# Performance work log

Hardware: AMD Instinct MI355X
Metric: run time of the kernel (lower is better)

The kernel has to match this reference:

```python
import jax, jax.numpy as jnp
import numpy as np

B, C, T = 16, 256, 8192
TF, HID, HEADS, HD, K = 512, 256, 8, 32, 2
EPS = 1e-6


def setup_inputs() -> dict:
    key = jax.random.key(0)
    ks = jax.random.split(key, 8)
    s = 0.02  # small init scale for weight matrices
    return {
        "x": jax.random.normal(ks[0], (B, C, 1, T), jnp.float32),
        "temb": jax.random.normal(ks[1], (B, TF), jnp.float32),
        "ln_w": jnp.ones((C,), jnp.float32),
        "ln_b": jnp.zeros((C,), jnp.float32),
        "ss_w": jax.random.normal(ks[2], (2 * C, TF), jnp.float32) * s,
        "ss_b": jnp.zeros((2 * C,), jnp.float32),
        "kv_w": jax.random.normal(ks[3], (2 * HID, C), jnp.float32) * s,
        "kv_b": jnp.zeros((2 * HID,), jnp.float32),
        "q": jax.random.normal(ks[4], (HEADS, HD), jnp.float32),
        "qt_w": jax.random.normal(ks[5], (HID, TF), jnp.float32) * s,
        "qt_b": jnp.zeros((HID,), jnp.float32),
        "rpe": jax.random.normal(ks[6], (HEADS, K), jnp.float32) * s,
        "proj_w": jax.random.normal(ks[7], (HID, HID), jnp.float32) * s,
        "proj_b": jnp.zeros((HID,), jnp.float32),
    }


def reference(x, temb, ln_w, ln_b, ss_w, ss_b, kv_w, kv_b, q, qt_w, qt_b, rpe, proj_w, proj_b):
    b, c, h, w = x.shape  # h == 1, w == T
    # --- LayerNorm2d: normalize over channel dim ---
    xt = jnp.transpose(x, (0, 2, 3, 1))  # [B,H,W,C]
    mu = jnp.mean(xt, axis=-1, keepdims=True)
    var = jnp.mean(jnp.square(xt - mu), axis=-1, keepdims=True)
    xn = (xt - mu) * jax.lax.rsqrt(var + EPS) * ln_w + ln_b
    xn = jnp.transpose(xn, (0, 3, 1, 2))  # [B,C,H,W]
    # --- ShiftAndScale (FiLM): SiLU -> Linear -> chunk ---
    cond = jax.nn.silu(temb) @ ss_w.T + ss_b  # [B, 2C]
    shift, scale = jnp.split(cond, 2, axis=1)
    xm = xn * (1.0 + scale[:, :, None, None]) + shift[:, :, None, None]
    # --- FusedQnA1d: learned-query windowed attention downsample (k=2, s=2) ---
    t = h * w
    t2 = t // K
    xf = xm.reshape(b, c, t)
    kv = jnp.einsum('bct,dc->bdt', xf, kv_w) + kv_b[None, :, None]  # [B,2*HID,T]
    kk, vv = jnp.split(kv, 2, axis=1)
    kk = kk.reshape(b, HEADS, HD, t2, K)  # non-overlapping stride-2 windows
    vv = vv.reshape(b, HEADS, HD, t2, K)
    # learned query, offset by timestep-conditioned query (use_timestep_query=True)
    qt = (jax.nn.silu(temb) @ qt_w.T + qt_b).reshape(b, HEADS, HD)
    qb = q[None] + qt  # [B,HEADS,HD]
    logits = jnp.einsum('bhd,bhdtw->bhtw', qb, kk) * (HD ** -0.5) + rpe[None, :, None, :]
    attn = jax.nn.softmax(logits, axis=-1)
    o = jnp.einsum('bhtw,bhdtw->bhdt', attn, vv).reshape(b, HID, t2)
    out = jnp.einsum('bct,dc->bdt', o, proj_w) + proj_b[None, :, None]
    return out.reshape(b, HID, h, w // K)
```

## Files before the change

### kernel.cpp

```cpp
#include <hip/hip_runtime.h>
#include <hip/hip_bf16.h>

#define Bn 16
#define Cn 256
#define Tn 8192
#define TFn 512
#define HIDn 256
#define HEADSn 8
#define HDn 32
#define T2n (Tn/2)
#define TW 256
#define T2W 128
#define XPAD 264
#define CKP 72

#define XSWZ(row) ((((row) >> 3) & 7) << 3)

#define WS_CS   0
#define WS_CC   4096
#define WS_CQ   8192
#define WS_G    12288
#define WS_H    16384
#define WS_QKB  20480
#define WS_QA   20608
#define WS_QH   20736
#define WS_AV   20864
#define WS_BV   24960
#define WS_BF16 29056
#define BF_QKW2 0
#define BF_WV2  65536
#define BF_PROJ 1114112

typedef __attribute__((ext_vector_type(8))) __bf16 bf16x8;
typedef __attribute__((ext_vector_type(4))) __bf16 bf16x4;
typedef __attribute__((ext_vector_type(4))) float f32x4;

__global__ __launch_bounds__(256)
void prepA_kernel(const float* __restrict__ temb,
                  const float* __restrict__ ss_w, const float* __restrict__ ss_b,
                  const float* __restrict__ qt_w, const float* __restrict__ qt_b,
                  const float* __restrict__ qw, float* __restrict__ ws)
{
    const int p = blockIdx.x;
    const int b = blockIdx.y;
    const int tid = threadIdx.x, lane = tid & 63, w = tid >> 6;
    __shared__ float st[TFn];
    for (int i = tid; i < TFn; i += 256) {
        float v = temb[b*TFn + i];
        st[i] = v / (1.f + __expf(-v));
    }
    __syncthreads();
    float4 s1 = *(const float4*)&st[lane*8];
    float4 s2 = *(const float4*)&st[lane*8 + 4];
    for (int i = 0; i < 16; ++i) {
        int row = p*64 + w*16 + i;
        const float* W = (row < 2*Cn) ? (ss_w + (size_t)row*TFn)
                                      : (qt_w + (size_t)(row - 2*Cn)*TFn);
        float4 a = *(const float4*)&W[lane*8];
        float4 c = *(const float4*)&W[lane*8 + 4];
        float d = a.x*s1.x + a.y*s1.y + a.z*s1.z + a.w*s1.w
                + c.x*s2.x + c.y*s2.y + c.z*s2.z + c.w*s2.w;
        #pragma unroll
        for (int off = 1; off < 64; off <<= 1) d += __shfl_xor(d, off);
        if (lane == 0) {
            if (row < Cn)
                ws[WS_CS + b*Cn + row] = d + ss_b[row];
            else if (row < 2*Cn)
                ws[WS_CC + b*Cn + (row - Cn)] = d + ss_b[row];
            else
                ws[WS_CQ + b*Cn + (row - 2*Cn)] = d + qt_b[row - 2*Cn] + qw[row - 2*Cn];
        }
    }
}

__global__ __launch_bounds__(256)
void prepB_kernel(const float* __restrict__ ln_w, const float* __restrict__ ln_b,
                  const float* __restrict__ kv_w, const float* __restrict__ kv_b,
                  float* __restrict__ ws)
{
    const int b = blockIdx.x, tid = threadIdx.x;
    __bf16* bfr = (__bf16*)(ws + WS_BF16);
    __shared__ float qbs[HIDn], gs[Cn], hs[Cn];
    __shared__ float pA[4][8], pH[4][8];
    const int c = tid, wv = tid >> 6, ln = tid & 63;

    float sc1 = 1.f + ws[WS_CC + b*Cn + c];
    float g = ln_w[c] * sc1;
    float h = ln_b[c] * sc1 + ws[WS_CS + b*Cn + c];
    gs[c] = g; hs[c] = h;
    ws[WS_G + b*Cn + c] = g;
    ws[WS_H + b*Cn + c] = h;
    qbs[c] = ws[WS_CQ + b*Cn + c];
    __syncthreads();

    __bf16* qkw2B = bfr + BF_QKW2 + b*16*Cn;
    for (int hh2 = 0; hh2 < HEADSn; ++hh2) {
        float accq = 0.f;
        #pragma unroll
        for (int d = 0; d < HDn; ++d)
            accq += qbs[hh2*HDn + d] * kv_w[(size_t)(hh2*HDn + d)*Cn + c];
        float wg = accq * gs[c];
        float wh = accq * hs[c];
        qkw2B[hh2*Cn + c] = (__bf16)wg;
        float ra = wg, rh = wh;
        #pragma unroll
        for (int off = 1; off < 64; off <<= 1) {
            ra += __shfl_xor(ra, off);
            rh += __shfl_xor(rh, off);
        }
        if (ln == 0) { pA[wv][hh2] = ra; pH[wv][hh2] = rh; }
    }
    for (int i = tid; i < 8*Cn; i += 256) qkw2B[8*Cn + i] = (__bf16)0.f;
    __syncthreads();
    if (tid < HEADSn) {
        ws[WS_QA + b*8 + tid] = pA[0][tid]+pA[1][tid]+pA[2][tid]+pA[3][tid];
        ws[WS_QH + b*8 + tid] = pH[0][tid]+pH[1][tid]+pH[2][tid]+pH[3][tid];
        float accb = 0.f;
        #pragma unroll
        for (int d = 0; d < HDn; ++d) accb += qbs[tid*HDn + d]*kv_b[tid*HDn + d];
        ws[WS_QKB + b*8 + tid] = accb;
    }
}

__global__ __launch_bounds__(256)
void prep2_kernel(const float* __restrict__ kv_w, const float* __restrict__ kv_b,
                  const float* __restrict__ proj_w, float* __restrict__ ws)
{
    const int tid = threadIdx.x, blk = blockIdx.x;
    __bf16* bfr = (__bf16*)(ws + WS_BF16);
    if (blk < 256) {
        int b  = blk >> 4, ch = blk & 15;
        int rr = tid >> 4, jj = tid & 15;
        int d  = ch*16 + rr;
        const float* gb = ws + WS_G + b*Cn;
        const float* hb = ws + WS_H + b*Cn;
        const float* wrow = kv_w + (size_t)(Cn + d)*Cn;
        __bf16* dst = bfr + BF_WV2 + (size_t)b*Cn*Cn + (size_t)d*Cn;
        float sa = 0.f, sb = 0.f;
        #pragma unroll
        for (int kk = 0; kk < 2; ++kk) {
            bf16x8 pk;
            #pragma unroll
            for (int j = 0; j < 8; ++j) {
                int cc = jj*16 + kk*8 + j;
                float v = wrow[cc], g = gb[cc];
                float vg = v*g;
                pk[j] = (__bf16)vg;
                sa += vg;
                sb += v*hb[cc];
            }
            *(bf16x8*)&dst[jj*16 + kk*8] = pk;
        }
        #pragma unroll
        for (int off = 1; off < 16; off <<= 1) {
            sa += __shfl_xor(sa, off);
            sb += __shfl_xor(sb, off);
        }
        if (jj == 0) {
            ws[WS_AV + b*Cn + d] = sa;
            ws[WS_BV + b*Cn + d] = sb + kv_b[Cn + d];
        }
    } else {
        size_t i0 = (size_t)(blk - 256)*4096 + (size_t)tid*16;
        #pragma unroll
        for (int kk = 0; kk < 2; ++kk) {
            bf16x8 pk;
            #pragma unroll
            for (int j = 0; j < 8; ++j) pk[j] = (__bf16)proj_w[i0 + kk*8 + j];
            *(bf16x8*)&bfr[BF_PROJ + i0 + kk*8] = pk;
        }
    }
}

__global__ __launch_bounds__(512, 2)
void qna_main(const float* __restrict__ x, const float* __restrict__ rpe,
              const float* __restrict__ proj_b,
              const float* __restrict__ ws, float* __restrict__ out)
{
    __shared__ __bf16 xcb[2][TW][CKP];
    __shared__ float spool[4096];
    __shared__ float ivs[TW], mivs[TW];
    __shared__ float AvS[Cn], BvS[Cn], pbs[Cn];
    __shared__ float qAs[8], qHs[8], qkbs2[8];
    __shared__ float rpes[8][2];

    const int tid  = threadIdx.x;
    const int bt   = blockIdx.x;
    const int b    = blockIdx.y;
    const int lane = tid & 63;
    const int w    = tid >> 6;
    const int r    = lane & 15;
    const int qq   = lane >> 4;

    const __bf16* bfr   = (const __bf16*)(ws + WS_BF16);
    const __bf16* qkw2B = bfr + BF_QKW2 + b*16*Cn;
    const __bf16* Wv2B  = bfr + BF_WV2 + (size_t)b*Cn*Cn;
    const __bf16* projB = bfr + BF_PROJ;

    if (tid < 256) {
        AvS[tid] = ws[WS_AV + b*Cn + tid];
        BvS[tid] = ws[WS_BV + b*Cn + tid];
    } else {
        int t2 = tid - 256;
        pbs[t2] = proj_b[t2];
        if (t2 < 8) {
            qAs[t2]   = ws[WS_QA + b*8 + t2];
            qHs[t2]   = ws[WS_QH + b*8 + t2];
            qkbs2[t2] = ws[WS_QKB + b*8 + t2];
        }
        if (t2 >= 16 && t2 < 32) rpes[(t2-16)>>1][t2&1] = rpe[t2-16];
    }

    const size_t xbase = (size_t)b*Cn*Tn + (size_t)bt*TW + 4*lane;
    const int tL = 4*lane;
    float4 v[8];
    float4 s4 = {0,0,0,0}, q4 = {0,0,0,0};

    auto stage_write = [&](int BUF) {
        #pragma unroll
        for (int i = 0; i < 8; ++i) {
            s4.x += v[i].x; s4.y += v[i].y; s4.z += v[i].z; s4.w += v[i].w;
            q4.x += v[i].x*v[i].x; q4.y += v[i].y*v[i].y;
            q4.z += v[i].z*v[i].z; q4.w += v[i].w*v[i].w;
        }
        #pragma unroll
        for (int j = 0; j < 4; ++j) {
            int t = tL + j;
            bf16x8 pk;
            pk[0]=(__bf16)((const float*)&v[0])[j]; pk[1]=(__bf16)((const float*)&v[1])[j];
            pk[2]=(__bf16)((const float*)&v[2])[j]; pk[3]=(__bf16)((const float*)&v[3])[j];
            pk[4]=(__bf16)((const float*)&v[4])[j]; pk[5]=(__bf16)((const float*)&v[5])[j];
            pk[6]=(__bf16)((const float*)&v[6])[j]; pk[7]=(__bf16)((const float*)&v[7])[j];
            *(bf16x8*)&xcb[BUF][t][(8*w) ^ XSWZ(t)] = pk;
        }
    };

    #pragma unroll
    for (int i = 0; i < 8; ++i)
        v[i] = *(const float4*)&x[xbase + (size_t)(8*w + i)*Tn];
    stage_write(0);
    __syncthreads();

    f32x4 accL[2];
    accL[0] = (f32x4){0.f,0.f,0.f,0.f};
    accL[1] = (f32x4){0.f,0.f,0.f,0.f};
    f32x4 acc[4][8];
    #pragma unroll
    for (int m = 0; m < 4; ++m)
        #pragma unroll
        for (int n = 0; n < 8; ++n) acc[m][n] = (f32x4){0.f,0.f,0.f,0.f};
    const int d0 = (w & 3) * 64;
    const int tb = (w >> 2) * 128;

    #pragma unroll
    for (int ch = 0; ch < 4; ++ch) {
        const int cur = ch & 1;
        if (ch < 3) {
            #pragma unroll
            for (int i = 0; i < 8; ++i)
                v[i] = *(const float4*)&x[xbase + (size_t)((ch+1)*64 + 8*w + i)*Tn];
        }
        #pragma unroll
        for (int k0 = 0; k0 < 2; ++k0) {
            const int kc = ch*64 + k0*32 + qq*8;
            const int cl = (k0*32 + qq*8);
            bf16x8 aQ = *(const bf16x8*)&qkw2B[(size_t)r*Cn + kc];
            #pragma unroll
            for (int u = 0; u < 2; ++u) {
                const int trow = (2*w + u)*16 + r;
                bf16x8 bq = *(const bf16x8*)&xcb[cur][trow][cl ^ XSWZ(trow)];
                accL[u] = __builtin_amdgcn_mfma_f32_16x16x32_bf16(aQ, bq, accL[u], 0, 0, 0);
            }
            bf16x8 bb[8];
            #pragma unroll
            for (int n = 0; n < 8; ++n) {
                const int row = tb + n*16 + r;
                bb[n] = *(const bf16x8*)&xcb[cur][row][cl ^ XSWZ(row)];
            }
            #pragma unroll
            for (int m = 0; m < 4; ++m) {
                bf16x8 a = *(const bf16x8*)&Wv2B[(size_t)(d0 + m*16 + r)*Cn + kc];
                #pragma unroll
                for (int n = 0; n < 8; ++n)
                    acc[m][n] = __builtin_amdgcn_mfma_f32_16x16x32_bf16(a, bb[n], acc[m][n], 0, 0, 0);
            }
        }
        if (ch < 3) {
            __syncthreads();
            stage_write(cur ^ 1);
            if (ch == 2) {
                spool[0*512 + w*64 + lane] = s4.x;
                spool[1*512 + w*64 + lane] = s4.y;
                spool[2*512 + w*64 + lane] = s4.z;
                spool[3*512 + w*64 + lane] = s4.w;
                spool[2048 + 0*512 + w*64 + lane] = q4.x;
                spool[2048 + 1*512 + w*64 + lane] = q4.y;
                spool[2048 + 2*512 + w*64 + lane] = q4.z;
                spool[2048 + 3*512 + w*64 + lane] = q4.w;
            }
            __syncthreads();
        }
    }

    __syncthreads();
    if (tid < 256) {
        const int t = tid, comp = t & 3, lq = t >> 2;
        float s = 0.f, sq = 0.f;
        #pragma unroll
        for (int w2 = 0; w2 < 8; ++w2) {
            s  += spool[comp*512 + w2*64 + lq];
            sq += spool[2048 + comp*512 + w2*64 + lq];
        }
        float mean = s * (1.f/Cn);
        float var  = sq * (1.f/Cn) - mean*mean;
        float iv   = rsqrtf(var + 1e-6f);
        ivs[t]  = iv;
        mivs[t] = mean * iv;
    }
    __syncthreads();

    float* aw = spool;
    {
        const float sc = 0.17677669529663687f;
        #pragma unroll
        for (int u = 0; u < 2; ++u) {
            const int tcol = (2*w + u)*16 + r;
            float iv = ivs[tcol], miv = mivs[tcol];
            #pragma unroll
            for (int rr = 0; rr < 4; ++rr) {
                int h  = (qq*4 + rr) & 7;
                float l = (accL[u][rr]*iv - miv*qAs[h] + qHs[h] + qkbs2[h])*sc + rpes[h][r&1];
                float mx = fmaxf(l, __shfl_xor(l, 1));
                float e  = __expf(l - mx);
                float sm = e + __shfl_xor(e, 1);
                float aval = e / sm;
                if (qq < 2) aw[(qq*4 + rr)*256 + tcol] = aval;
            }
        }
    }
    __syncthreads();

    __bf16* oTp = &xcb[0][0][0];
    {
        #pragma unroll
        for (int m = 0; m < 4; ++m) {
            const int dbase = d0 + m*16 + qq*4;
            const int h = dbase >> 5;
            float av4[4], bv4[4];
            #pragma unroll
            for (int rr = 0; rr < 4; ++rr) { av4[rr] = AvS[dbase+rr]; bv4[rr] = BvS[dbase+rr]; }
            #pragma unroll
            for (int n = 0; n < 8; ++n) {
                const int tl = tb + n*16 + r;
                float ivn = ivs[tl], mivn = mivs[tl];
                float a0 = aw[h*256 + (tl & ~1)], a1 = aw[h*256 + (tl | 1)];
                bf16x4 ov;
                #pragma unroll
                for (int rr = 0; rr < 4; ++rr) {
                    float vv = ivn*acc[m][n][rr] - mivn*av4[rr] + bv4[rr];
                    float vo = __shfl_xor(vv, 1);
                    float o  = a0*vv + a1*vo;
                    ov[rr] = (__bf16)o;
                }
                if (!(r & 1)) {
                    int u = (tb >> 1) + n*8 + (r >> 1);
                    *(bf16x4*)&oTp[(size_t)u*XPAD + dbase] = ov;
                }
            }
        }
    }
    __syncthreads();

    const int t2b = (w >> 2) * 64;
    f32x4 acc2[4][4];
    #pragma unroll
    for (int m = 0; m < 4; ++m)
        #pragma unroll
        for (int n = 0; n < 4; ++n) acc2[m][n] = (f32x4){0.f,0.f,0.f,0.f};
    #pragma unroll
    for (int k0 = 0; k0 < 8; ++k0) {
        bf16x8 bb2[4];
        #pragma unroll
        for (int n = 0; n < 4; ++n)
            bb2[n] = *(const bf16x8*)&oTp[(size_t)(t2b + n*16 + r)*XPAD + k0*32 + qq*8];
        #pragma unroll
        for (int m = 0; m < 4; ++m) {
            bf16x8 a = *(const bf16x8*)&projB[(size_t)(d0 + m*16 + r)*Cn + k0*32 + qq*8];
            #pragma unroll
            for (int n = 0; n < 4; ++n)
                acc2[m][n] = __builtin_amdgcn_mfma_f32_16x16x32_bf16(a, bb2[n], acc2[m][n], 0, 0, 0);
        }
    }

    {
        float* ob = out + (size_t)b*HIDn*T2n + (size_t)bt*T2W;
        #pragma unroll
        for (int m = 0; m < 4; ++m) {
            #pragma unroll
            for (int n = 0; n < 4; ++n) {
                #pragma unroll
                for (int rr = 0; rr < 4; ++rr) {
                    int e = d0 + m*16 + qq*4 + rr;
                    ob[(size_t)e*T2n + t2b + n*16 + r] = acc2[m][n][rr] + pbs[e];
                }
            }
        }
    }
}

extern "C" void kernel_launch(void* const* d_in, const int* in_sizes, int n_in,
                              void* d_out, int out_size, void* d_ws, size_t ws_size,
                              hipStream_t stream) {
    (void)in_sizes; (void)n_in; (void)out_size; (void)ws_size;
    const float* x      = (const float*)d_in[0];
    const float* temb   = (const float*)d_in[1];
    const float* ln_w   = (const float*)d_in[2];
    const float* ln_b   = (const float*)d_in[3];
    const float* ss_w   = (const float*)d_in[4];
    const float* ss_b   = (const float*)d_in[5];
    const float* kv_w   = (const float*)d_in[6];
    const float* kv_b   = (const float*)d_in[7];
    const float* q      = (const float*)d_in[8];
    const float* qt_w   = (const float*)d_in[9];
    const float* qt_b   = (const float*)d_in[10];
    const float* rpe    = (const float*)d_in[11];
    const float* proj_w = (const float*)d_in[12];
    const float* proj_b = (const float*)d_in[13];
    float* ws  = (float*)d_ws;
    float* out = (float*)d_out;

    prepA_kernel<<<dim3(12, Bn), dim3(256), 0, stream>>>(
        temb, ss_w, ss_b, qt_w, qt_b, q, ws);
    prepB_kernel<<<dim3(Bn), dim3(256), 0, stream>>>(ln_w, ln_b, kv_w, kv_b, ws);
    prep2_kernel<<<dim3(272), dim3(256), 0, stream>>>(kv_w, kv_b, proj_w, ws);
    qna_main<<<dim3(Tn/TW, Bn), dim3(512), 0, stream>>>(x, rpe, proj_b, ws, out);
}
```

Measured before the change: 111.6 us.

## Split fused attention kernel into stage-1 and projection kernels via workspace

```diff
diff --git a/kernel.cpp b/kernel.cpp
--- a/kernel.cpp
+++ b/kernel.cpp
@@ -13,8 +13,10 @@
 #define T2W 128
 #define XPAD 264
 #define CKP 72
-
-#define XSWZ(row) ((((row) >> 3) & 7) << 3)
+#define S1TW 128
+
+#define XSWZ(row)   ((((row) >> 3) & 7) << 3)
+#define XSWZ32(row) ((((row) >> 3) & 3) << 3)
 
 #define WS_CS   0
 #define WS_CC   4096
@@ -30,6 +32,8 @@
 #define BF_QKW2 0
 #define BF_WV2  65536
 #define BF_PROJ 1114112
+#define WS_OG   618880
+#define WS_NEED 36029952ull
 
 typedef __attribute__((ext_vector_type(8))) __bf16 bf16x8;
 typedef __attribute__((ext_vector_type(4))) __bf16 bf16x4;
@@ -168,6 +172,244 @@
             #pragma unroll
             for (int j = 0; j < 8; ++j) pk[j] = (__bf16)proj_w[i0 + kk*8 + j];
             *(bf16x8*)&bfr[BF_PROJ + i0 + kk*8] = pk;
+        }
+    }
+}
+
+__global__ __launch_bounds__(256, 2)
+void qna_stage1(const float* __restrict__ x, const float* __restrict__ rpe,
+                float* __restrict__ ws)
+{
+    __shared__ __bf16 xcb[2][S1TW][40];
+    __shared__ float sp_s[4*128], sp_q[4*128];
+    __shared__ float ivs[S1TW], mivs[S1TW];
+    __shared__ float aw[8*128];
+    __shared__ __bf16 oTb[64][264];
+    __shared__ float AvS[Cn], BvS[Cn];
+    __shared__ float qAs[8], qHs[8], qkbs2[8];
+    __shared__ float rpes[8][2];
+
+    const int tid  = threadIdx.x;
+    const int bt   = blockIdx.x;
+    const int b    = blockIdx.y;
+    const int lane = tid & 63;
+    const int w    = tid >> 6;
+    const int r    = lane & 15;
+    const int qq   = lane >> 4;
+
+    const __bf16* bfr   = (const __bf16*)(ws + WS_BF16);
+    const __bf16* qkw2B = bfr + BF_QKW2 + b*16*Cn;
+    const __bf16* Wv2B  = bfr + BF_WV2 + (size_t)b*Cn*Cn;
+    __bf16* oG = (__bf16*)(ws + WS_OG) + ((size_t)b*T2n + (size_t)bt*64)*Cn;
+
+    AvS[tid] = ws[WS_AV + b*Cn + tid];
+    BvS[tid] = ws[WS_BV + b*Cn + tid];
+    if (tid < 8) {
+        qAs[tid]   = ws[WS_QA + b*8 + tid];
+        qHs[tid]   = ws[WS_QH + b*8 + tid];
+        qkbs2[tid] = ws[WS_QKB + b*8 + tid];
+    }
+    if (tid >= 16 && tid < 32) rpes[(tid-16)>>1][tid&1] = rpe[tid-16];
+
+    const size_t xbase = (size_t)b*Cn*Tn + (size_t)bt*S1TW + 2*lane;
+    const int t0 = 2*lane;
+    float2 v[8];
+    float s0 = 0.f, s1 = 0.f, q0 = 0.f, q1 = 0.f;
+
+    auto stage_write = [&](int BUF) {
+        bf16x8 p0, p1;
+        #pragma unroll
+        for (int i = 0; i < 8; ++i) {
+            s0 += v[i].x; q0 += v[i].x*v[i].x;
+            s1 += v[i].y; q1 += v[i].y*v[i].y;
+            p0[i] = (__bf16)v[i].x;
+            p1[i] = (__bf16)v[i].y;
+        }
+        *(bf16x8*)&xcb[BUF][t0][(8*w) ^ XSWZ32(t0)]     = p0;
+        *(bf16x8*)&xcb[BUF][t0+1][(8*w) ^ XSWZ32(t0+1)] = p1;
+    };
+
+    #pragma unroll
+    for (int i = 0; i < 8; ++i)
+        v[i] = *(const float2*)&x[xbase + (size_t)(8*w + i)*Tn];
+    stage_write(0);
+    __syncthreads();
+
+    f32x4 accL[2];
+    accL[0] = (f32x4){0.f,0.f,0.f,0.f};
+    accL[1] = (f32x4){0.f,0.f,0.f,0.f};
+    f32x4 acc[4][8];
+    #pragma unroll
+    for (int m = 0; m < 4; ++m)
+        #pragma unroll
+        for (int n = 0; n < 8; ++n) acc[m][n] = (f32x4){0.f,0.f,0.f,0.f};
+    const int d0 = w * 64;
+
+    #pragma unroll
+    for (int ch = 0; ch < 8; ++ch) {
+        const int cur = ch & 1;
+        if (ch < 7) {
+            #pragma unroll
+            for (int i = 0; i < 8; ++i)
+                v[i] = *(const float2*)&x[xbase + (size_t)((ch+1)*32 + 8*w + i)*Tn];
+        }
+        const int kc = ch*32 + qq*8;
+        const int cl = qq*8;
+        {
+            bf16x8 aQ = *(const bf16x8*)&qkw2B[(size_t)r*Cn + kc];
+            #pragma unroll
+            for (int u = 0; u < 2; ++u) {
+                const int trow = (2*w + u)*16 + r;
+                bf16x8 bq = *(const bf16x8*)&xcb[cur][trow][cl ^ XSWZ32(trow)];
+                accL[u] = __builtin_amdgcn_mfma_f32_16x16x32_bf16(aQ, bq, accL[u], 0, 0, 0);
+            }
+        }
+        {
+            bf16x8 bb[8];
+            #pragma unroll
+            for (int n = 0; n < 8; ++n) {
+                const int row = n*16 + r;
+                bb[n] = *(const bf16x8*)&xcb[cur][row][cl ^ XSWZ32(row)];
+            }
+            #pragma unroll
+            for (int m = 0; m < 4; ++m) {
+                bf16x8 a = *(const bf16x8*)&Wv2B[(size_t)(d0 + m*16 + r)*Cn + kc];
+                #pragma unroll
+                for (int n = 0; n < 8; ++n)
+                    acc[m][n] = __builtin_amdgcn_mfma_f32_16x16x32_bf16(a, bb[n], acc[m][n], 0, 0, 0);
+            }
+        }
+        if (ch < 7) {
+            __syncthreads();
+            stage_write(cur ^ 1);
+            if (ch == 6) {
+                sp_s[w*128 + t0]     = s0;
+                sp_s[w*128 + t0 + 1] = s1;
+                sp_q[w*128 + t0]     = q0;
+                sp_q[w*128 + t0 + 1] = q1;
+            }
+            __syncthreads();
+        }
+    }
+
+    if (tid < S1TW) {
+        float s = sp_s[tid] + sp_s[128+tid] + sp_s[256+tid] + sp_s[384+tid];
+        float sq = sp_q[tid] + sp_q[128+tid] + sp_q[256+tid] + sp_q[384+tid];
+        float mean = s * (1.f/Cn);
+        float var  = sq * (1.f/Cn) - mean*mean;
+        float iv   = rsqrtf(var + 1e-6f);
+        ivs[tid]  = iv;
+        mivs[tid] = mean * iv;
+    }
+    __syncthreads();
+
+    {
+        const float sc = 0.17677669529663687f;
+        #pragma unroll
+        for (int u = 0; u < 2; ++u) {
+            const int tcol = (2*w + u)*16 + r;
+            float iv = ivs[tcol], miv = mivs[tcol];
+            #pragma unroll
+            for (int rr = 0; rr < 4; ++rr) {
+                int h  = (qq*4 + rr) & 7;
+                float l = (accL[u][rr]*iv - miv*qAs[h] + qHs[h] + qkbs2[h])*sc + rpes[h][r&1];
+                float mx = fmaxf(l, __shfl_xor(l, 1));
+                float e  = __expf(l - mx);
+                float sm = e + __shfl_xor(e, 1);
+                float aval = e / sm;
+                if (qq < 2) aw[(qq*4 + rr)*128 + tcol] = aval;
+            }
+        }
+    }
+    __syncthreads();
+
+    {
+        #pragma unroll
+        for (int m = 0; m < 4; ++m) {
+            const int dbase = d0 + m*16 + qq*4;
+            const int h = dbase >> 5;
+            float av4[4], bv4[4];
+            #pragma unroll
+            for (int rr = 0; rr < 4; ++rr) { av4[rr] = AvS[dbase+rr]; bv4[rr] = BvS[dbase+rr]; }
+            #pragma unroll
+            for (int n = 0; n < 8; ++n) {
+                const int tl = n*16 + r;
+                float ivn = ivs[tl], mivn = mivs[tl];
+                float a0 = aw[h*128 + (tl & ~1)], a1 = aw[h*128 + (tl | 1)];
+                bf16x4 ov;
+                #pragma unroll
+                for (int rr = 0; rr < 4; ++rr) {
+                    float vv = ivn*acc[m][n][rr] - mivn*av4[rr] + bv4[rr];
+                    float vo = __shfl_xor(vv, 1);
+                    float o  = a0*vv + a1*vo;
+                    ov[rr] = (__bf16)o;
+                }
+                if (!(r & 1)) {
+                    int u = n*8 + (r >> 1);
+                    *(bf16x4*)&oTb[u][dbase] = ov;
+                }
+            }
+        }
+    }
+    __syncthreads();
+
+    {
+        int u = tid >> 2, seg = tid & 3;
+        const __bf16* src = &oTb[u][seg*64];
+        __bf16* dst = oG + (size_t)u*Cn + seg*64;
+        #pragma unroll
+        for (int k = 0; k < 8; ++k)
+            *(bf16x8*)&dst[k*8] = *(const bf16x8*)&src[k*8];
+    }
+}
+
+__global__ __launch_bounds__(256, 2)
+void qna_proj(const float* __restrict__ ws, const float* __restrict__ proj_b,
+              float* __restrict__ out)
+{
+    const int tid  = threadIdx.x;
+    const int bt   = blockIdx.x;
+    const int b    = blockIdx.y;
+    const int lane = tid & 63;
+    const int w    = tid >> 6;
+    const int r    = lane & 15;
+    const int qq   = lane >> 4;
+
+    const __bf16* projB = (const __bf16*)(ws + WS_BF16) + BF_PROJ;
+    const __bf16* oG = (const __bf16*)(ws + WS_OG) + ((size_t)b*T2n + (size_t)bt*128)*Cn;
+    const int e0 = w * 64;
+
+    f32x4 acc[4][8];
+    #pragma unroll
+    for (int m = 0; m < 4; ++m)
+        #pragma unroll
+        for (int n = 0; n < 8; ++n) acc[m][n] = (f32x4){0.f,0.f,0.f,0.f};
+
+    #pragma unroll
+    for (int k0 = 0; k0 < 8; ++k0) {
+        bf16x8 bb[8];
+        #pragma unroll
+        for (int n = 0; n < 8; ++n)
+            bb[n] = *(const bf16x8*)&oG[(size_t)(n*16 + r)*Cn + k0*32 + qq*8];
+        #pragma unroll
+        for (int m = 0; m < 4; ++m) {
+            bf16x8 a = *(const bf16x8*)&projB[(size_t)(e0 + m*16 + r)*Cn + k0*32 + qq*8];
+            #pragma unroll
+            for (int n = 0; n < 8; ++n)
+                acc[m][n] = __builtin_amdgcn_mfma_f32_16x16x32_bf16(a, bb[n], acc[m][n], 0, 0, 0);
+        }
+    }
+
+    float* ob = out + (size_t)b*HIDn*T2n + (size_t)bt*128;
+    #pragma unroll
+    for (int m = 0; m < 4; ++m) {
+        #pragma unroll
+        for (int rr = 0; rr < 4; ++rr) {
+            int e = e0 + m*16 + qq*4 + rr;
+            float pb = proj_b[e];
+            #pragma unroll
+            for (int n = 0; n < 8; ++n)
+                ob[(size_t)e*T2n + n*16 + r] = acc[m][n][rr] + pb;
         }
     }
 }
@@ -411,7 +653,7 @@
 extern "C" void kernel_launch(void* const* d_in, const int* in_sizes, int n_in,
                               void* d_out, int out_size, void* d_ws, size_t ws_size,
                               hipStream_t stream) {
-    (void)in_sizes; (void)n_in; (void)out_size; (void)ws_size;
+    (void)in_sizes; (void)n_in; (void)out_size;
     const float* x      = (const float*)d_in[0];
     const float* temb   = (const float*)d_in[1];
     const float* ln_w   = (const float*)d_in[2];
@@ -433,5 +675,11 @@
         temb, ss_w, ss_b, qt_w, qt_b, q, ws);
     prepB_kernel<<<dim3(Bn), dim3(256), 0, stream>>>(ln_w, ln_b, kv_w, kv_b, ws);
     prep2_kernel<<<dim3(272), dim3(256), 0, stream>>>(kv_w, kv_b, proj_w, ws);
-    qna_main<<<dim3(Tn/TW, Bn), dim3(512), 0, stream>>>(x, rpe, proj_b, ws, out);
+
+    if (ws_size >= WS_NEED) {
+        qna_stage1<<<dim3(Tn/S1TW, Bn), dim3(256), 0, stream>>>(x, rpe, ws);
+        qna_proj<<<dim3(T2n/128, Bn), dim3(256), 0, stream>>>(ws, proj_b, out);
+    } else {
+        qna_main<<<dim3(Tn/TW, Bn), dim3(512), 0, stream>>>(x, rpe, proj_b, ws, out);
+    }
 }
```

New measurement: 148.9 us. +33.4%, slower.

## Deepen x-load prefetch to two chunks and halve per-chunk barriers

Applied to the files above, without the earlier changes.

```diff
diff --git a/kernel.cpp b/kernel.cpp
--- a/kernel.cpp
+++ b/kernel.cpp
@@ -213,32 +213,59 @@
 
     const size_t xbase = (size_t)b*Cn*Tn + (size_t)bt*TW + 4*lane;
     const int tL = 4*lane;
-    float4 v[8];
+    float4 vA[4], vB[4];
     float4 s4 = {0,0,0,0}, q4 = {0,0,0,0};
 
-    auto stage_write = [&](int BUF) {
-        #pragma unroll
-        for (int i = 0; i < 8; ++i) {
-            s4.x += v[i].x; s4.y += v[i].y; s4.z += v[i].z; s4.w += v[i].w;
-            q4.x += v[i].x*v[i].x; q4.y += v[i].y*v[i].y;
-            q4.z += v[i].z*v[i].z; q4.w += v[i].w*v[i].w;
+    auto issueA = [&](int ch) {
+        #pragma unroll
+        for (int i = 0; i < 4; ++i)
+            vA[i] = *(const float4*)&x[xbase + (size_t)(ch*64 + 8*w + i)*Tn];
+    };
+    auto issueB = [&](int ch) {
+        #pragma unroll
+        for (int i = 0; i < 4; ++i)
+            vB[i] = *(const float4*)&x[xbase + (size_t)(ch*64 + 8*w + 4 + i)*Tn];
+    };
+    auto stageA = [&](int BUF) {
+        #pragma unroll
+        for (int i = 0; i < 4; ++i) {
+            s4.x += vA[i].x; s4.y += vA[i].y; s4.z += vA[i].z; s4.w += vA[i].w;
+            q4.x += vA[i].x*vA[i].x; q4.y += vA[i].y*vA[i].y;
+            q4.z += vA[i].z*vA[i].z; q4.w += vA[i].w*vA[i].w;
         }
         #pragma unroll
         for (int j = 0; j < 4; ++j) {
             int t = tL + j;
-            bf16x8 pk;
-            pk[0]=(__bf16)((const float*)&v[0])[j]; pk[1]=(__bf16)((const float*)&v[1])[j];
-            pk[2]=(__bf16)((const float*)&v[2])[j]; pk[3]=(__bf16)((const float*)&v[3])[j];
-            pk[4]=(__bf16)((const float*)&v[4])[j]; pk[5]=(__bf16)((const float*)&v[5])[j];
-            pk[6]=(__bf16)((const float*)&v[6])[j]; pk[7]=(__bf16)((const float*)&v[7])[j];
-            *(bf16x8*)&xcb[BUF][t][(8*w) ^ XSWZ(t)] = pk;
+            bf16x4 pk;
+            pk[0] = (__bf16)((const float*)&vA[0])[j];
+            pk[1] = (__bf16)((const float*)&vA[1])[j];
+            pk[2] = (__bf16)((const float*)&vA[2])[j];
+            pk[3] = (__bf16)((const float*)&vA[3])[j];
+            *(bf16x4*)&xcb[BUF][t][(8*w) ^ XSWZ(t)] = pk;
         }
     };
-
-    #pragma unroll
-    for (int i = 0; i < 8; ++i)
-        v[i] = *(const float4*)&x[xbase + (size_t)(8*w + i)*Tn];
-    stage_write(0);
+    auto stageB = [&](int BUF) {
+        #pragma unroll
+        for (int i = 0; i < 4; ++i) {
+            s4.x += vB[i].x; s4.y += vB[i].y; s4.z += vB[i].z; s4.w += vB[i].w;
+            q4.x += vB[i].x*vB[i].x; q4.y += vB[i].y*vB[i].y;
+            q4.z += vB[i].z*vB[i].z; q4.w += vB[i].w*vB[i].w;
+        }
+        #pragma unroll
+        for (int j = 0; j < 4; ++j) {
+            int t = tL + j;
+            bf16x4 pk;
+            pk[0] = (__bf16)((const float*)&vB[0])[j];
+            pk[1] = (__bf16)((const float*)&vB[1])[j];
+            pk[2] = (__bf16)((const float*)&vB[2])[j];
+            pk[3] = (__bf16)((const float*)&vB[3])[j];
+            *(bf16x4*)&xcb[BUF][t][((8*w) ^ XSWZ(t)) + 4] = pk;
+        }
+    };
+
+    issueA(0); issueB(0);
+    stageA(0); stageB(0);
+    issueA(1); issueB(1);
     __syncthreads();
 
     f32x4 accL[2];
@@ -256,38 +283,10 @@
     for (int ch = 0; ch < 4; ++ch) {
         const int cur = ch & 1;
         if (ch < 3) {
-            #pragma unroll
-            for (int i = 0; i < 8; ++i)
-                v[i] = *(const float4*)&x[xbase + (size_t)((ch+1)*64 + 8*w + i)*Tn];
-        }
-        #pragma unroll
-        for (int k0 = 0; k0 < 2; ++k0) {
-            const int kc = ch*64 + k0*32 + qq*8;
-            const int cl = (k0*32 + qq*8);
-            bf16x8 aQ = *(const bf16x8*)&qkw2B[(size_t)r*Cn + kc];
-            #pragma unroll
-            for (int u = 0; u < 2; ++u) {
-                const int trow = (2*w + u)*16 + r;
-                bf16x8 bq = *(const bf16x8*)&xcb[cur][trow][cl ^ XSWZ(trow)];
-                accL[u] = __builtin_amdgcn_mfma_f32_16x16x32_bf16(aQ, bq, accL[u], 0, 0, 0);
-            }
-            bf16x8 bb[8];
-            #pragma unroll
-            for (int n = 0; n < 8; ++n) {
-                const int row = tb + n*16 + r;
-                bb[n] = *(const bf16x8*)&xcb[cur][row][cl ^ XSWZ(row)];
-            }
-            #pragma unroll
-            for (int m = 0; m < 4; ++m) {
-                bf16x8 a = *(const bf16x8*)&Wv2B[(size_t)(d0 + m*16 + r)*Cn + kc];
-                #pragma unroll
-                for (int n = 0; n < 8; ++n)
-                    acc[m][n] = __builtin_amdgcn_mfma_f32_16x16x32_bf16(a, bb[n], acc[m][n], 0, 0, 0);
-            }
-        }
-        if (ch < 3) {
-            __syncthreads();
-            stage_write(cur ^ 1);
+            stageA(cur ^ 1);
+            if (ch < 2) issueA(ch + 2);
+            stageB(cur ^ 1);
+            if (ch < 2) issueB(ch + 2);
             if (ch == 2) {
                 spool[0*512 + w*64 + lane] = s4.x;
                 spool[1*512 + w*64 + lane] = s4.y;
@@ -298,11 +297,35 @@
                 spool[2048 + 2*512 + w*64 + lane] = q4.z;
                 spool[2048 + 3*512 + w*64 + lane] = q4.w;
             }
-            __syncthreads();
-        }
-    }
-
-    __syncthreads();
+        }
+        #pragma unroll
+        for (int k0 = 0; k0 < 2; ++k0) {
+            const int kc = ch*64 + k0*32 + qq*8;
+            const int cl = k0*32 + qq*8;
+            bf16x8 aQ = *(const bf16x8*)&qkw2B[(size_t)r*Cn + kc];
+            #pragma unroll
+            for (int u = 0; u < 2; ++u) {
+                const int trow = (2*w + u)*16 + r;
+                bf16x8 bq = *(const bf16x8*)&xcb[cur][trow][cl ^ XSWZ(trow)];
+                accL[u] = __builtin_amdgcn_mfma_f32_16x16x32_bf16(aQ, bq, accL[u], 0, 0, 0);
+            }
+            bf16x8 bb[8];
+            #pragma unroll
+            for (int n = 0; n < 8; ++n) {
+                const int row = tb + n*16 + r;
+                bb[n] = *(const bf16x8*)&xcb[cur][row][cl ^ XSWZ(row)];
+            }
+            #pragma unroll
+            for (int m = 0; m < 4; ++m) {
+                bf16x8 a = *(const bf16x8*)&Wv2B[(size_t)(d0 + m*16 + r)*Cn + kc];
+                #pragma unroll
+                for (int n = 0; n < 8; ++n)
+                    acc[m][n] = __builtin_amdgcn_mfma_f32_16x16x32_bf16(a, bb[n], acc[m][n], 0, 0, 0);
+            }
+        }
+        if (ch < 3) __syncthreads();
+    }
+
     if (tid < 256) {
         const int t = tid, comp = t & 3, lq = t >> 2;
         float s = 0.f, sq = 0.f;
```

Result: slower. 128.9 us (+15.5%).
